# Kernel optimization log

Measured on AMD Instinct MI355X. Metric: run time of the kernel, lower is better.

Reference implementation:

```python
import jax, jax.numpy as jnp
import numpy as np

B, N = 65536, 128

def setup_inputs() -> dict:
    key = jax.random.key(0)
    k1, k2, k3, k4, k5 = jax.random.split(key, 5)
    density = jax.random.uniform(k1, (B, N), dtype=jnp.float32) * 10.0   # nonneg densities
    deltas = jax.random.uniform(k2, (B, N), dtype=jnp.float32) * 0.05 + 1e-3  # positive step sizes
    zs = jnp.cumsum(deltas, axis=-1) + 2.0                               # monotone sample depths
    raw_rgbs = jax.random.uniform(k4, (B, N, 3), dtype=jnp.float32)
    raw_normals = jax.random.normal(k5, (B, N, 3), dtype=jnp.float32)
    return {"density": density, "deltas": deltas, "zs": zs,
            "raw_rgbs": raw_rgbs, "raw_normals": raw_normals}


def reference(density, deltas, zs, raw_rgbs, raw_normals):
    # alpha -> transmittance (exclusive cumprod) -> weight
    alpha = 1.0 - jnp.exp(-density * deltas)                 # [B, N]
    one_minus = 1.0 - alpha
    cp = jnp.cumprod(one_minus, axis=-1)                     # inclusive cumprod
    trans = jnp.concatenate([jnp.ones_like(cp[:, :1]), cp[:, :-1]], axis=-1)  # exclusive
    weight = alpha * trans                                   # [B, N]

    # composites
    rgb = jnp.einsum('bn,bnc->bc', weight, raw_rgbs)         # [B, 3]
    acc = jnp.sum(weight, axis=1, keepdims=True)             # [B, 1]
    depth = jnp.sum(weight * zs, axis=1, keepdims=True) / (acc + 1e-8)  # normalized
    normal = jnp.einsum('bn,bnc->bc', weight, raw_normals)   # [B, 3]

    # pack outputs: rgb(3) | depth(1) | normal(3) | acc(1) -> [B, 8]
    return jnp.concatenate([rgb, depth, normal, acc], axis=-1)
```

## Files before the change

### kernel.cpp

```cpp
#include <hip/hip_runtime.h>


constexpr int RAYS = 65536;
constexpr int NS   = 128;

#define DPP_ADD(x, ctrl, rm)                                                   \
    x += __int_as_float(__builtin_amdgcn_update_dpp(                           \
        0, __float_as_int(x), ctrl, rm, 0xf, true))

__device__ __forceinline__ float scan32(float x) {
    DPP_ADD(x, 0x111, 0xf);
    DPP_ADD(x, 0x112, 0xf);
    DPP_ADD(x, 0x114, 0xf);
    DPP_ADD(x, 0x118, 0xf);
    DPP_ADD(x, 0x142, 0xa);
    return x;
}

__global__ __launch_bounds__(256) void render_composite_kernel(
    const float* __restrict__ density,
    const float* __restrict__ deltas,
    const float* __restrict__ zs,
    const float* __restrict__ rgbs,
    const float* __restrict__ normals,
    float* __restrict__ out)
{
    const int tid  = threadIdx.x;
    const int lane = tid & 63;
    const int k    = lane & 31;
    const int ray  = blockIdx.x * 8 + (tid >> 6) * 2 + (lane >> 5);

    const size_t row  = (size_t)ray * NS;
    const size_t row3 = (size_t)ray * NS * 3;

    const float4 d  = reinterpret_cast<const float4*>(density + row)[k];
    const float4 dl = reinterpret_cast<const float4*>(deltas  + row)[k];
    const float4 z  = reinterpret_cast<const float4*>(zs      + row)[k];

    const float4* rg = reinterpret_cast<const float4*>(rgbs    + row3) + k * 3;
    const float4* nm = reinterpret_cast<const float4*>(normals + row3) + k * 3;
    const float4 r0 = rg[0], r1 = rg[1], r2 = rg[2];
    const float4 n0 = nm[0], n1 = nm[1], n2 = nm[2];

    const float s0 = d.x * dl.x;
    const float s1 = d.y * dl.y;
    const float s2 = d.z * dl.z;
    const float s3 = d.w * dl.w;
    const float slocal = (s0 + s1) + (s2 + s3);

    const float prefix = scan32(slocal);
    const float S0 = prefix - slocal;
    const float S1 = S0 + s0;
    const float S2 = S1 + s1;
    const float S3 = S2 + s2;
    const float S4 = S3 + s3;

    const float e0 = __expf(-S0);
    const float e1 = __expf(-S1);
    const float e2 = __expf(-S2);
    const float e3 = __expf(-S3);
    const float e4 = __expf(-S4);
    const float w0 = e0 - e1;
    const float w1 = e1 - e2;
    const float w2 = e2 - e3;
    const float w3 = e3 - e4;

    float acc_r  = w0 * r0.x + w1 * r0.w + w2 * r1.z + w3 * r2.y;
    float acc_g  = w0 * r0.y + w1 * r1.x + w2 * r1.w + w3 * r2.z;
    float acc_b  = w0 * r0.z + w1 * r1.y + w2 * r2.x + w3 * r2.w;
    float acc_nr = w0 * n0.x + w1 * n0.w + w2 * n1.z + w3 * n2.y;
    float acc_ng = w0 * n0.y + w1 * n1.x + w2 * n1.w + w3 * n2.z;
    float acc_nb = w0 * n0.z + w1 * n1.y + w2 * n2.x + w3 * n2.w;
    float acc_w  = (w0 + w1) + (w2 + w3);
    float acc_wz = w0 * z.x + w1 * z.y + w2 * z.z + w3 * z.w;

    acc_r  = scan32(acc_r);
    acc_g  = scan32(acc_g);
    acc_b  = scan32(acc_b);
    acc_nr = scan32(acc_nr);
    acc_ng = scan32(acc_ng);
    acc_nb = scan32(acc_nb);
    acc_w  = scan32(acc_w);
    acc_wz = scan32(acc_wz);

    if (k == 31) {
        const float depth = acc_wz / (acc_w + 1e-8f);
        float4* o = reinterpret_cast<float4*>(out + (size_t)ray * 8);
        o[0] = make_float4(acc_r, acc_g, acc_b, depth);
        o[1] = make_float4(acc_nr, acc_ng, acc_nb, acc_w);
    }
}

extern "C" void kernel_launch(void* const* d_in, const int* in_sizes, int n_in,
                              void* d_out, int out_size, void* d_ws, size_t ws_size,
                              hipStream_t stream) {
    const float* density = (const float*)d_in[0];
    const float* deltas  = (const float*)d_in[1];
    const float* zs      = (const float*)d_in[2];
    const float* rgbs    = (const float*)d_in[3];
    const float* normals = (const float*)d_in[4];
    float* out = (float*)d_out;

    const int grid = RAYS / 8;
    render_composite_kernel<<<grid, 256, 0, stream>>>(
        density, deltas, zs, rgbs, normals, out);
}
```

Measured before the change: 278.9 us.

## Coalesce rgb/normal loads across wave and redistribute weights via LDS

Changes the rgb and normal loads from a per-lane stride-3 float4 pattern to fully contiguous wave-wide float4 loads covering two rays. Per-sample weights are written to shared memory so each lane can fetch the weights matching the channel elements it loaded. Partial sums are then merged across the two halves of the wave before the final scan. This aims at better global memory coalescing, at the cost of LDS traffic, extra select logic and more cross-lane shuffles.

```diff
diff --git a/kernel.cpp b/kernel.cpp
--- a/kernel.cpp
+++ b/kernel.cpp
@@ -3,6 +3,7 @@
 
 constexpr int RAYS = 65536;
 constexpr int NS   = 128;
+constexpr int WPB  = 4;
 
 #define DPP_ADD(x, ctrl, rm)                                                   \
     x += __int_as_float(__builtin_amdgcn_update_dpp(                           \
@@ -25,69 +26,118 @@
     const float* __restrict__ normals,
     float* __restrict__ out)
 {
+    __shared__ __align__(16) float wlds[WPB][256];
+
     const int tid  = threadIdx.x;
-    const int lane = tid & 63;
-    const int k    = lane & 31;
-    const int ray  = blockIdx.x * 8 + (tid >> 6) * 2 + (lane >> 5);
+    const int wv   = tid >> 6;
+    const int l    = tid & 63;
+    const int k    = l & 31;
+    const int half = l >> 5;
 
-    const size_t row  = (size_t)ray * NS;
-    const size_t row3 = (size_t)ray * NS * 3;
+    const int ray0 = (blockIdx.x * WPB + wv) * 2;
+    const int ray  = ray0 + half;
 
+    const size_t row = (size_t)ray * NS;
     const float4 d  = reinterpret_cast<const float4*>(density + row)[k];
     const float4 dl = reinterpret_cast<const float4*>(deltas  + row)[k];
     const float4 z  = reinterpret_cast<const float4*>(zs      + row)[k];
 
-    const float4* rg = reinterpret_cast<const float4*>(rgbs    + row3) + k * 3;
-    const float4* nm = reinterpret_cast<const float4*>(normals + row3) + k * 3;
-    const float4 r0 = rg[0], r1 = rg[1], r2 = rg[2];
-    const float4 n0 = nm[0], n1 = nm[1], n2 = nm[2];
+    const float4* cr = reinterpret_cast<const float4*>(rgbs)    + (size_t)ray0 * 96;
+    const float4* cn = reinterpret_cast<const float4*>(normals) + (size_t)ray0 * 96;
+    const float4 vr0 = cr[0 * 64 + l];
+    const float4 vr1 = cr[1 * 64 + l];
+    const float4 vr2 = cr[2 * 64 + l];
+    const float4 vn0 = cn[0 * 64 + l];
+    const float4 vn1 = cn[1 * 64 + l];
+    const float4 vn2 = cn[2 * 64 + l];
 
     const float s0 = d.x * dl.x;
     const float s1 = d.y * dl.y;
     const float s2 = d.z * dl.z;
     const float s3 = d.w * dl.w;
     const float slocal = (s0 + s1) + (s2 + s3);
-
     const float prefix = scan32(slocal);
     const float S0 = prefix - slocal;
-    const float S1 = S0 + s0;
-    const float S2 = S1 + s1;
-    const float S3 = S2 + s2;
-    const float S4 = S3 + s3;
 
     const float e0 = __expf(-S0);
-    const float e1 = __expf(-S1);
-    const float e2 = __expf(-S2);
-    const float e3 = __expf(-S3);
-    const float e4 = __expf(-S4);
-    const float w0 = e0 - e1;
-    const float w1 = e1 - e2;
-    const float w2 = e2 - e3;
-    const float w3 = e3 - e4;
+    const float e1 = __expf(-(S0 + s0));
+    const float e2 = __expf(-(S0 + s0 + s1));
+    const float e3 = __expf(-(S0 + s0 + s1 + s2));
+    const float e4 = __expf(-(S0 + slocal));
+    const float w0 = e0 - e1, w1 = e1 - e2, w2 = e2 - e3, w3 = e3 - e4;
 
-    float acc_r  = w0 * r0.x + w1 * r0.w + w2 * r1.z + w3 * r2.y;
-    float acc_g  = w0 * r0.y + w1 * r1.x + w2 * r1.w + w3 * r2.z;
-    float acc_b  = w0 * r0.z + w1 * r1.y + w2 * r2.x + w3 * r2.w;
-    float acc_nr = w0 * n0.x + w1 * n0.w + w2 * n1.z + w3 * n2.y;
-    float acc_ng = w0 * n0.y + w1 * n1.x + w2 * n1.w + w3 * n2.z;
-    float acc_nb = w0 * n0.z + w1 * n1.y + w2 * n2.x + w3 * n2.w;
     float acc_w  = (w0 + w1) + (w2 + w3);
     float acc_wz = w0 * z.x + w1 * z.y + w2 * z.z + w3 * z.w;
 
-    acc_r  = scan32(acc_r);
-    acc_g  = scan32(acc_g);
-    acc_b  = scan32(acc_b);
-    acc_nr = scan32(acc_nr);
-    acc_ng = scan32(acc_ng);
-    acc_nb = scan32(acc_nb);
+    reinterpret_cast<float4*>(&wlds[wv][0])[l] = make_float4(w0, w1, w2, w3);
+    const float* wbase = &wlds[wv][0];
+
+    float r0c0 = 0.f, r0c1 = 0.f, r0c2 = 0.f;
+    float r1c0 = 0.f, r1c1 = 0.f, r1c2 = 0.f;
+    float m0c0 = 0.f, m0c1 = 0.f, m0c2 = 0.f;
+    float m1c0 = 0.f, m1c1 = 0.f, m1c2 = 0.f;
+
+    auto proc = [](const float4 v, float wA, float wB, int rt,
+                   float& c0, float& c1, float& c2) {
+        const float q0 = wA * v.x + wB * v.w;
+        const float q1 = ((rt == 2) ? wB : wA) * v.y;
+        const float q2 = ((rt >= 1) ? wB : wA) * v.z;
+        const float a0 = (rt == 0) ? q0 : (rt == 1) ? q2 : q1;
+        const float a1 = (rt == 0) ? q1 : (rt == 1) ? q0 : q2;
+        const float a2 = (rt == 0) ? q2 : (rt == 1) ? q1 : q0;
+        c0 += a0; c1 += a1; c2 += a2;
+    };
+
+    #pragma unroll
+    for (int t = 0; t < 3; ++t) {
+        const int f  = 256 * t + 4 * l;
+        const int q  = f / 3;
+        const int rt = f - 3 * q;
+        const float wA = wbase[q];
+        const float wB = wbase[q + 1];
+        const float4 vr = (t == 0) ? vr0 : (t == 1) ? vr1 : vr2;
+        const float4 vn = (t == 0) ? vn0 : (t == 1) ? vn1 : vn2;
+
+        if (t == 0) {
+            proc(vr, wA, wB, rt, r0c0, r0c1, r0c2);
+            proc(vn, wA, wB, rt, m0c0, m0c1, m0c2);
+        } else if (t == 2) {
+            proc(vr, wA, wB, rt, r1c0, r1c1, r1c2);
+            proc(vn, wA, wB, rt, m1c0, m1c1, m1c2);
+        } else {
+            float t0 = 0.f, t1c = 0.f, t2c = 0.f, u0 = 0.f, u1 = 0.f, u2 = 0.f;
+            proc(vr, wA, wB, rt, t0, t1c, t2c);
+            proc(vn, wA, wB, rt, u0, u1, u2);
+            const bool isr0 = (l < 32);
+            r0c0 += isr0 ? t0 : 0.f;  r1c0 += isr0 ? 0.f : t0;
+            r0c1 += isr0 ? t1c : 0.f; r1c1 += isr0 ? 0.f : t1c;
+            r0c2 += isr0 ? t2c : 0.f; r1c2 += isr0 ? 0.f : t2c;
+            m0c0 += isr0 ? u0 : 0.f;  m1c0 += isr0 ? 0.f : u0;
+            m0c1 += isr0 ? u1 : 0.f;  m1c1 += isr0 ? 0.f : u1;
+            m0c2 += isr0 ? u2 : 0.f;  m1c2 += isr0 ? 0.f : u2;
+        }
+    }
+
+    auto reduce2 = [&](float cR0, float cR1) -> float {
+        const float sel = half ? cR1 : cR0;
+        const float oth = half ? cR0 : cR1;
+        const float m = sel + __shfl_xor(oth, 32, 64);
+        return scan32(m);
+    };
+    const float R  = reduce2(r0c0, r1c0);
+    const float G  = reduce2(r0c1, r1c1);
+    const float Bc = reduce2(r0c2, r1c2);
+    const float NR = reduce2(m0c0, m1c0);
+    const float NG = reduce2(m0c1, m1c1);
+    const float NB = reduce2(m0c2, m1c2);
     acc_w  = scan32(acc_w);
     acc_wz = scan32(acc_wz);
 
     if (k == 31) {
         const float depth = acc_wz / (acc_w + 1e-8f);
         float4* o = reinterpret_cast<float4*>(out + (size_t)ray * 8);
-        o[0] = make_float4(acc_r, acc_g, acc_b, depth);
-        o[1] = make_float4(acc_nr, acc_ng, acc_nb, acc_w);
+        o[0] = make_float4(R, G, Bc, depth);
+        o[1] = make_float4(NR, NG, NB, acc_w);
     }
 }
 
@@ -101,7 +151,7 @@
     const float* normals = (const float*)d_in[4];
     float* out = (float*)d_out;
 
-    const int grid = RAYS / 8;
+    const int grid = RAYS / (WPB * 2);
     render_composite_kernel<<<grid, 256, 0, stream>>>(
         density, deltas, zs, rgbs, normals, out);
 }
```

Result: no change. 279.7 us (+0.3%).
